# Kernel optimization log

Hardware: AMD Instinct MI355X
Metric: run time of the kernel (lower is better)

Reference implementation:

```python
import jax, jax.numpy as jnp
import numpy as np

NUM_ITERATIONS = 3
EPS = 1e-08

def squash(s, axis=-1):
    norm = jnp.linalg.norm(s, axis=axis, keepdims=True)
    scale = norm ** 2 / (1 + norm ** 2)
    return scale * s / (norm + EPS)

def setup_inputs() -> dict:
    key = jax.random.key(0)
    k1, k2 = jax.random.split(key)
    B, C, M, O, I = 256, 1152, 8, 16, 8
    u = jax.random.normal(k1, (B, C, I), dtype=jnp.float32)
    W = jax.random.normal(k2, (C, M, O, I), dtype=jnp.float32)
    return {"u": u, "W": W}

def reference(u, W):
    B, C, I = u.shape
    M, O = W.shape[1], W.shape[2]
    # u_hat: [B, C, M, O] -- predicted output capsule vectors
    u_hat = jnp.einsum('cmoi,bci->bcmo', W, u)
    b = jnp.zeros((B, C, M), dtype=u.dtype)
    v = None
    for r in range(NUM_ITERATIONS):
        c = jax.nn.softmax(b, axis=2)  # softmax over emotion dim
        s = jnp.einsum('bcm,bcmo->bmo', c, u_hat)
        v = squash(s)  # [B, M, O]
        if r < NUM_ITERATIONS - 1:
            uv = jnp.einsum('bcmo,bmo->bcm', u_hat, v)
            b = b + uv
    return v
```

## Files before the change

### kernel.cpp

```cpp
#include <hip/hip_runtime.h>

#define B_SZ 256
#define C_SZ 1152
#define MO   128
#define CSPL 32
#define CRNG (C_SZ / CSPL)
#define CAPS_EPS 1e-8f

struct alignas(8) H4 { _Float16 h[4]; };
union PK2 { unsigned int u32; _Float16 h[2]; };

__global__ __launch_bounds__(256) void caps_uhat(
    const float* __restrict__ u,
    const float* __restrict__ W,
    unsigned int* __restrict__ uhat)
{
    const int bid = blockIdx.x;
    const int c   = (bid & 7) * 144 + (bid >> 3);
    const int tid = threadIdx.x;
    const int l   = tid & 63;
    const int wv  = tid >> 6;

    __shared__ __align__(16) float u_sh[B_SZ][8];

    const float4* wp =
        reinterpret_cast<const float4*>(W + (size_t)c * 1024) + l * 4;
    const float4 wa = wp[0], wb = wp[1], wc4 = wp[2], wd = wp[3];

    {
        const float4* up = reinterpret_cast<const float4*>(
            u + ((size_t)tid * C_SZ + c) * 8);
        float4 a0 = up[0], a1 = up[1];
        *reinterpret_cast<float4*>(&u_sh[tid][0]) = a0;
        *reinterpret_cast<float4*>(&u_sh[tid][4]) = a1;
    }
    __syncthreads();

    unsigned int* ub = uhat + (size_t)c * B_SZ * 64 + l;
    const int b0 = wv * 64;

    for (int bb = 0; bb < 64; bb += 8) {
#pragma unroll
        for (int k = 0; k < 8; ++k) {
            const int b = b0 + bb + k;
            const float4 u0 = *reinterpret_cast<const float4*>(&u_sh[b][0]);
            const float4 u1 = *reinterpret_cast<const float4*>(&u_sh[b][4]);
            float h0 = wa.x*u0.x + wa.y*u0.y + wa.z*u0.z + wa.w*u0.w
                     + wb.x*u1.x + wb.y*u1.y + wb.z*u1.z + wb.w*u1.w;
            float h1 = wc4.x*u0.x + wc4.y*u0.y + wc4.z*u0.z + wc4.w*u0.w
                     + wd.x*u1.x + wd.y*u1.y + wd.z*u1.z + wd.w*u1.w;
            PK2 pk;
            pk.h[0] = (_Float16)h0;
            pk.h[1] = (_Float16)h1;
            ub[(size_t)b * 64] = pk.u32;
        }
    }
}

__global__ __launch_bounds__(128) void caps_vcalc(
    const float* __restrict__ part_in,
    const float* __restrict__ addv,
    float* __restrict__ vout)
{
    const int b = blockIdx.x, t = threadIdx.x;
    float s = 0.f;
#pragma unroll
    for (int k = 0; k < CSPL; ++k)
        s += part_in[((size_t)k * B_SZ + b) * MO + t];
    float n2 = s * s;
    n2 += __shfl_xor(n2, 1);
    n2 += __shfl_xor(n2, 2);
    n2 += __shfl_xor(n2, 4);
    n2 += __shfl_xor(n2, 8);
    float norm = sqrtf(n2);
    float v = (n2 / (1.f + n2)) * s / (norm + CAPS_EPS);
    if (addv) v += addv[(size_t)b * MO + t];
    vout[(size_t)b * MO + t] = v;
}

template <bool UNIF>
__global__ __launch_bounds__(256) void caps_route(
    const H4* __restrict__ uhat,
    const float* __restrict__ vbuf,
    float* __restrict__ part_out)
{
    const int bt  = blockIdx.x & 31;
    const int csp = blockIdx.x >> 5;
    const int tid = threadIdx.x;
    const int g   = tid >> 5;
    const int l   = tid & 31;
    const int b   = bt * 8 + g;
    const int mo4 = l * 4;

    float4 v4 = make_float4(0.f, 0.f, 0.f, 0.f);
    if (!UNIF)
        v4 = *reinterpret_cast<const float4*>(vbuf + (size_t)b * MO + mo4);
    float acc[4] = {0.f, 0.f, 0.f, 0.f};

    const int cbeg = csp * CRNG, cend = cbeg + CRNG;
    const H4* base = uhat + (size_t)b * 32 + l;

    H4 r0 = base[(size_t)cbeg * B_SZ * 32];
    H4 r1 = base[(size_t)(cbeg + 1) * B_SZ * 32];

    for (int c = cbeg; c < cend; c += 2) {
        H4 n0 = r0, n1 = r1;
        if (c + 2 < cend) {
            n0 = base[(size_t)(c + 2) * B_SZ * 32];
            n1 = base[(size_t)(c + 3) * B_SZ * 32];
        }
#pragma unroll
        for (int q = 0; q < 2; ++q) {
            H4 r = q ? r1 : r0;
            float uh0 = (float)r.h[0], uh1 = (float)r.h[1];
            float uh2 = (float)r.h[2], uh3 = (float)r.h[3];
            float cw;
            if (UNIF) {
                cw = 0.125f;
            } else {
                float uv = uh0 * v4.x + uh1 * v4.y + uh2 * v4.z + uh3 * v4.w;
                uv += __shfl_xor(uv, 1);
                uv += __shfl_xor(uv, 2);
                float mx = fmaxf(uv, __shfl_xor(uv, 4));
                mx = fmaxf(mx, __shfl_xor(mx, 8));
                mx = fmaxf(mx, __shfl_xor(mx, 16));
                float e = expf(uv - mx);
                float den = e;
                den += __shfl_xor(den, 4);
                den += __shfl_xor(den, 8);
                den += __shfl_xor(den, 16);
                cw = e / den;
            }
            acc[0] = fmaf(cw, uh0, acc[0]);
            acc[1] = fmaf(cw, uh1, acc[1]);
            acc[2] = fmaf(cw, uh2, acc[2]);
            acc[3] = fmaf(cw, uh3, acc[3]);
        }
        r0 = n0; r1 = n1;
    }
    *reinterpret_cast<float4*>(part_out + ((size_t)csp * B_SZ + b) * MO + mo4) =
        make_float4(acc[0], acc[1], acc[2], acc[3]);
}

template <int R>
__global__ __launch_bounds__(256) void caps_small(
    const float* __restrict__ u, const float* __restrict__ W,
    const float* __restrict__ s_in, const float* __restrict__ v0_in,
    float* __restrict__ s_out, float* __restrict__ v0_out,
    float* __restrict__ out)
{
    const int b = blockIdx.x, tid = threadIdx.x;
    __shared__ float sh_v[8][17];
    __shared__ float sh_part[256][17];

    if (R >= 1) {
        if (tid < 128) {
            float val = s_in[b * 128 + tid];
            float n2 = val * val;
            n2 += __shfl_xor(n2, 1); n2 += __shfl_xor(n2, 2);
            n2 += __shfl_xor(n2, 4); n2 += __shfl_xor(n2, 8);
            float norm = sqrtf(n2);
            float v = (n2 / (1.f + n2)) * val / (norm + CAPS_EPS);
            int m = tid >> 4, o = tid & 15;
            if (R == 1) { v0_out[b * 128 + tid] = v; sh_v[m][o] = v; }
            else        { sh_v[m][o] = v + v0_in[b * 128 + tid]; }
        }
        __syncthreads();
    }
    const int c_local = tid >> 3, m = tid & 7;
    float s_acc[16];
#pragma unroll
    for (int o = 0; o < 16; ++o) s_acc[o] = 0.f;
    for (int cc = 0; cc < C_SZ; cc += 32) {
        const int c = cc + c_local;
        const float4* up = reinterpret_cast<const float4*>(
            u + (size_t)(b * C_SZ + c) * 8);
        float4 u0 = up[0], u1 = up[1];
        float u8[8] = {u0.x, u0.y, u0.z, u0.w, u1.x, u1.y, u1.z, u1.w};
        float uh[16];
        const float4* wp = reinterpret_cast<const float4*>(
            W + (size_t)((c * 8 + m) * 16) * 8);
#pragma unroll
        for (int o = 0; o < 16; ++o) {
            float4 w0 = wp[o * 2], w1 = wp[o * 2 + 1];
            uh[o] = w0.x * u8[0] + w0.y * u8[1] + w0.z * u8[2] + w0.w * u8[3] +
                    w1.x * u8[4] + w1.y * u8[5] + w1.z * u8[6] + w1.w * u8[7];
        }
        float cw;
        if (R == 0) cw = 0.125f;
        else {
            float uv = 0.f;
#pragma unroll
            for (int o = 0; o < 16; ++o) uv = fmaf(uh[o], sh_v[m][o], uv);
            float mx = uv;
            mx = fmaxf(mx, __shfl_xor(mx, 1));
            mx = fmaxf(mx, __shfl_xor(mx, 2));
            mx = fmaxf(mx, __shfl_xor(mx, 4));
            float e = expf(uv - mx);
            float den = e;
            den += __shfl_xor(den, 1); den += __shfl_xor(den, 2);
            den += __shfl_xor(den, 4);
            cw = e / den;
        }
#pragma unroll
        for (int o = 0; o < 16; ++o) s_acc[o] = fmaf(cw, uh[o], s_acc[o]);
    }
#pragma unroll
    for (int o = 0; o < 16; ++o) sh_part[tid][o] = s_acc[o];
    __syncthreads();
    if (tid < 128) {
        const int m2 = tid >> 4, o2 = tid & 15;
        float s = 0.f;
#pragma unroll
        for (int gg = 0; gg < 32; ++gg) s += sh_part[gg * 8 + m2][o2];
        if (R < 2) s_out[b * 128 + tid] = s;
        else {
            float n2 = s * s;
            n2 += __shfl_xor(n2, 1); n2 += __shfl_xor(n2, 2);
            n2 += __shfl_xor(n2, 4); n2 += __shfl_xor(n2, 8);
            float norm = sqrtf(n2);
            out[b * 128 + tid] = (n2 / (1.f + n2)) * s / (norm + CAPS_EPS);
        }
    }
}

extern "C" void kernel_launch(void* const* d_in, const int* in_sizes, int n_in,
                              void* d_out, int out_size, void* d_ws, size_t ws_size,
                              hipStream_t stream) {
    const float* u = (const float*)d_in[0];
    const float* W = (const float*)d_in[1];
    float* out = (float*)d_out;

    const size_t UHAT_BYTES  = (size_t)C_SZ * B_SZ * MO * 2;
    const size_t PART_FLOATS = (size_t)CSPL * B_SZ * MO;
    const size_t NEED = UHAT_BYTES + 2 * PART_FLOATS * 4 + 2 * B_SZ * MO * 4;

    if (ws_size >= NEED) {
        unsigned int* uhat_w = (unsigned int*)d_ws;
        const H4* uhat_r = (const H4*)d_ws;
        float* partA = (float*)((char*)d_ws + UHAT_BYTES);
        float* partB = partA + PART_FLOATS;
        float* v0    = partB + PART_FLOATS;
        float* vsum  = v0 + B_SZ * MO;

        dim3 gridU(C_SZ), gridR(CSPL * 32), blk(256);
        caps_uhat<<<gridU, blk, 0, stream>>>(u, W, uhat_w);
        caps_route<true ><<<gridR, blk, 0, stream>>>(uhat_r, nullptr, partA);
        caps_vcalc<<<dim3(B_SZ), dim3(128), 0, stream>>>(partA, nullptr, v0);
        caps_route<false><<<gridR, blk, 0, stream>>>(uhat_r, v0, partB);
        caps_vcalc<<<dim3(B_SZ), dim3(128), 0, stream>>>(partB, v0, vsum);
        caps_route<false><<<gridR, blk, 0, stream>>>(uhat_r, vsum, partA);
        caps_vcalc<<<dim3(B_SZ), dim3(128), 0, stream>>>(partA, nullptr, out);
    } else {
        float* sA = (float*)d_ws;
        float* sB = sA + 32768;
        float* v0 = sB + 32768;
        dim3 grid(B_SZ), blk(256);
        caps_small<0><<<grid, blk, 0, stream>>>(u, W, nullptr, nullptr, sA, nullptr, nullptr);
        caps_small<1><<<grid, blk, 0, stream>>>(u, W, sA, nullptr, sB, v0, nullptr);
        caps_small<2><<<grid, blk, 0, stream>>>(u, W, sB, v0, nullptr, nullptr, out);
    }
}
```

Measured before the change: 86.34 us.

## Fuse first uniform routing pass into u_hat computation kernel

```diff
diff --git a/kernel.cpp b/kernel.cpp
--- a/kernel.cpp
+++ b/kernel.cpp
@@ -3,48 +3,64 @@
 #define B_SZ 256
 #define C_SZ 1152
 #define MO   128
+#define CAPS_EPS 1e-8f
+
+#define USPL 72
+#define UCPB 16
+#define UCPW 4
+#define UBPB 8
 #define CSPL 32
 #define CRNG (C_SZ / CSPL)
-#define CAPS_EPS 1e-8f
 
 struct alignas(8) H4 { _Float16 h[4]; };
 union PK2 { unsigned int u32; _Float16 h[2]; };
 
-__global__ __launch_bounds__(256) void caps_uhat(
+__global__ __launch_bounds__(256, 4) void caps_uhat_f(
     const float* __restrict__ u,
     const float* __restrict__ W,
-    unsigned int* __restrict__ uhat)
+    unsigned int* __restrict__ uhat,
+    float* __restrict__ part0)
 {
     const int bid = blockIdx.x;
-    const int c   = (bid & 7) * 144 + (bid >> 3);
+    const int csp = bid >> 5;
+    const int bt  = bid & 31;
+    const int c0  = csp * UCPB;
+    const int b0  = bt * UBPB;
     const int tid = threadIdx.x;
     const int l   = tid & 63;
     const int wv  = tid >> 6;
 
-    __shared__ __align__(16) float u_sh[B_SZ][8];
-
-    const float4* wp =
-        reinterpret_cast<const float4*>(W + (size_t)c * 1024) + l * 4;
-    const float4 wa = wp[0], wb = wp[1], wc4 = wp[2], wd = wp[3];
-
-    {
+    __shared__ __align__(16) float u_sh[UBPB][UCPB][8];
+    __shared__ __align__(16) float s_lds[4][UBPB][MO];
+
+    if (tid < 128) {
+        const int bb = tid >> 4, cl = tid & 15;
         const float4* up = reinterpret_cast<const float4*>(
-            u + ((size_t)tid * C_SZ + c) * 8);
-        float4 a0 = up[0], a1 = up[1];
-        *reinterpret_cast<float4*>(&u_sh[tid][0]) = a0;
-        *reinterpret_cast<float4*>(&u_sh[tid][4]) = a1;
+            u + ((size_t)(b0 + bb) * C_SZ + c0 + cl) * 8);
+        *reinterpret_cast<float4*>(&u_sh[bb][cl][0]) = up[0];
+        *reinterpret_cast<float4*>(&u_sh[bb][cl][4]) = up[1];
     }
     __syncthreads();
 
-    unsigned int* ub = uhat + (size_t)c * B_SZ * 64 + l;
-    const int b0 = wv * 64;
-
-    for (int bb = 0; bb < 64; bb += 8) {
-#pragma unroll
-        for (int k = 0; k < 8; ++k) {
-            const int b = b0 + bb + k;
-            const float4 u0 = *reinterpret_cast<const float4*>(&u_sh[b][0]);
-            const float4 u1 = *reinterpret_cast<const float4*>(&u_sh[b][4]);
+    float acc[UBPB][2];
+#pragma unroll
+    for (int bb = 0; bb < UBPB; ++bb) { acc[bb][0] = 0.f; acc[bb][1] = 0.f; }
+
+#pragma unroll
+    for (int k = 0; k < UCPW; ++k) {
+        const int cl = wv * UCPW + k;
+        const int c  = c0 + cl;
+        const float4* wp =
+            reinterpret_cast<const float4*>(W + (size_t)c * 1024) + l * 4;
+        const float4 wa = wp[0], wb = wp[1], wc4 = wp[2], wd = wp[3];
+
+        unsigned int* ub = uhat + (size_t)c * B_SZ * 64 + l;
+#pragma unroll
+        for (int bb = 0; bb < UBPB; ++bb) {
+            const float4 u0 =
+                *reinterpret_cast<const float4*>(&u_sh[bb][cl][0]);
+            const float4 u1 =
+                *reinterpret_cast<const float4*>(&u_sh[bb][cl][4]);
             float h0 = wa.x*u0.x + wa.y*u0.y + wa.z*u0.z + wa.w*u0.w
                      + wb.x*u1.x + wb.y*u1.y + wb.z*u1.z + wb.w*u1.w;
             float h1 = wc4.x*u0.x + wc4.y*u0.y + wc4.z*u0.z + wc4.w*u0.w
@@ -52,20 +68,41 @@
             PK2 pk;
             pk.h[0] = (_Float16)h0;
             pk.h[1] = (_Float16)h1;
-            ub[(size_t)b * 64] = pk.u32;
-        }
+            ub[(size_t)(b0 + bb) * 64] = pk.u32;
+            acc[bb][0] += h0;
+            acc[bb][1] += h1;
+        }
+    }
+
+#pragma unroll
+    for (int bb = 0; bb < UBPB; ++bb)
+        *reinterpret_cast<float2*>(&s_lds[wv][bb][2 * l]) =
+            make_float2(acc[bb][0] * 0.125f, acc[bb][1] * 0.125f);
+    __syncthreads();
+
+    {
+        const int bb = tid >> 5, j = tid & 31;
+        float4 r = make_float4(0.f, 0.f, 0.f, 0.f);
+#pragma unroll
+        for (int w = 0; w < 4; ++w) {
+            const float4 x =
+                *reinterpret_cast<const float4*>(&s_lds[w][bb][4 * j]);
+            r.x += x.x; r.y += x.y; r.z += x.z; r.w += x.w;
+        }
+        *reinterpret_cast<float4*>(
+            part0 + ((size_t)csp * B_SZ + b0 + bb) * MO + 4 * j) = r;
     }
 }
 
 __global__ __launch_bounds__(128) void caps_vcalc(
     const float* __restrict__ part_in,
     const float* __restrict__ addv,
-    float* __restrict__ vout)
+    float* __restrict__ vout,
+    int nsplit)
 {
     const int b = blockIdx.x, t = threadIdx.x;
     float s = 0.f;
-#pragma unroll
-    for (int k = 0; k < CSPL; ++k)
+    for (int k = 0; k < nsplit; ++k)
         s += part_in[((size_t)k * B_SZ + b) * MO + t];
     float n2 = s * s;
     n2 += __shfl_xor(n2, 1);
@@ -78,7 +115,6 @@
     vout[(size_t)b * MO + t] = v;
 }
 
-template <bool UNIF>
 __global__ __launch_bounds__(256) void caps_route(
     const H4* __restrict__ uhat,
     const float* __restrict__ vbuf,
@@ -92,9 +128,8 @@
     const int b   = bt * 8 + g;
     const int mo4 = l * 4;
 
-    float4 v4 = make_float4(0.f, 0.f, 0.f, 0.f);
-    if (!UNIF)
-        v4 = *reinterpret_cast<const float4*>(vbuf + (size_t)b * MO + mo4);
+    const float4 v4 =
+        *reinterpret_cast<const float4*>(vbuf + (size_t)b * MO + mo4);
     float acc[4] = {0.f, 0.f, 0.f, 0.f};
 
     const int cbeg = csp * CRNG, cend = cbeg + CRNG;
@@ -114,23 +149,18 @@
             H4 r = q ? r1 : r0;
             float uh0 = (float)r.h[0], uh1 = (float)r.h[1];
             float uh2 = (float)r.h[2], uh3 = (float)r.h[3];
-            float cw;
-            if (UNIF) {
-                cw = 0.125f;
-            } else {
-                float uv = uh0 * v4.x + uh1 * v4.y + uh2 * v4.z + uh3 * v4.w;
-                uv += __shfl_xor(uv, 1);
-                uv += __shfl_xor(uv, 2);
-                float mx = fmaxf(uv, __shfl_xor(uv, 4));
-                mx = fmaxf(mx, __shfl_xor(mx, 8));
-                mx = fmaxf(mx, __shfl_xor(mx, 16));
-                float e = expf(uv - mx);
-                float den = e;
-                den += __shfl_xor(den, 4);
-                den += __shfl_xor(den, 8);
-                den += __shfl_xor(den, 16);
-                cw = e / den;
-            }
+            float uv = uh0 * v4.x + uh1 * v4.y + uh2 * v4.z + uh3 * v4.w;
+            uv += __shfl_xor(uv, 1);
+            uv += __shfl_xor(uv, 2);
+            float mx = fmaxf(uv, __shfl_xor(uv, 4));
+            mx = fmaxf(mx, __shfl_xor(mx, 8));
+            mx = fmaxf(mx, __shfl_xor(mx, 16));
+            float e = expf(uv - mx);
+            float den = e;
+            den += __shfl_xor(den, 4);
+            den += __shfl_xor(den, 8);
+            den += __shfl_xor(den, 16);
+            float cw = e / den;
             acc[0] = fmaf(cw, uh0, acc[0]);
             acc[1] = fmaf(cw, uh1, acc[1]);
             acc[2] = fmaf(cw, uh2, acc[2]);
@@ -231,26 +261,28 @@
     const float* W = (const float*)d_in[1];
     float* out = (float*)d_out;
 
-    const size_t UHAT_BYTES  = (size_t)C_SZ * B_SZ * MO * 2;
-    const size_t PART_FLOATS = (size_t)CSPL * B_SZ * MO;
-    const size_t NEED = UHAT_BYTES + 2 * PART_FLOATS * 4 + 2 * B_SZ * MO * 4;
+    const size_t UHAT_BYTES = (size_t)C_SZ * B_SZ * MO * 2;
+    const size_t P0_FLOATS  = (size_t)USPL * B_SZ * MO;
+    const size_t PR_FLOATS  = (size_t)CSPL * B_SZ * MO;
+    const size_t NEED = UHAT_BYTES +
+                        (P0_FLOATS + 2 * PR_FLOATS + 2 * B_SZ * MO) * 4;
 
     if (ws_size >= NEED) {
         unsigned int* uhat_w = (unsigned int*)d_ws;
         const H4* uhat_r = (const H4*)d_ws;
-        float* partA = (float*)((char*)d_ws + UHAT_BYTES);
-        float* partB = partA + PART_FLOATS;
-        float* v0    = partB + PART_FLOATS;
+        float* part0 = (float*)((char*)d_ws + UHAT_BYTES);
+        float* partA = part0 + P0_FLOATS;
+        float* partB = partA + PR_FLOATS;
+        float* v0    = partB + PR_FLOATS;
         float* vsum  = v0 + B_SZ * MO;
 
-        dim3 gridU(C_SZ), gridR(CSPL * 32), blk(256);
-        caps_uhat<<<gridU, blk, 0, stream>>>(u, W, uhat_w);
-        caps_route<true ><<<gridR, blk, 0, stream>>>(uhat_r, nullptr, partA);
-        caps_vcalc<<<dim3(B_SZ), dim3(128), 0, stream>>>(partA, nullptr, v0);
-        caps_route<false><<<gridR, blk, 0, stream>>>(uhat_r, v0, partB);
-        caps_vcalc<<<dim3(B_SZ), dim3(128), 0, stream>>>(partB, v0, vsum);
-        caps_route<false><<<gridR, blk, 0, stream>>>(uhat_r, vsum, partA);
-        caps_vcalc<<<dim3(B_SZ), dim3(128), 0, stream>>>(partA, nullptr, out);
+        dim3 blk(256);
+        caps_uhat_f<<<dim3(USPL * 32), blk, 0, stream>>>(u, W, uhat_w, part0);
+        caps_vcalc<<<dim3(B_SZ), dim3(128), 0, stream>>>(part0, nullptr, v0, USPL);
+        caps_route<<<dim3(CSPL * 32), blk, 0, stream>>>(uhat_r, v0, partA);
+        caps_vcalc<<<dim3(B_SZ), dim3(128), 0, stream>>>(partA, v0, vsum, CSPL);
+        caps_route<<<dim3(CSPL * 32), blk, 0, stream>>>(uhat_r, vsum, partB);
+        caps_vcalc<<<dim3(B_SZ), dim3(128), 0, stream>>>(partB, nullptr, out, CSPL);
     } else {
         float* sA = (float*)d_ws;
         float* sB = sA + 32768;
```

Result: slower. 103.1 us (+19.4%).
